# Optimization experiments

Hardware: AMD Instinct MI355X
Metric: run time of the kernel (lower is better)

The kernel has to match this reference:

```python
import jax, jax.numpy as jnp
import numpy as np

N_QUBITS = 256
N_LAYERS = 8
BATCH = 65536


def _ln(h, w, b):
    mu = jnp.mean(h, axis=-1, keepdims=True)
    var = jnp.mean((h - mu) ** 2, axis=-1, keepdims=True)
    return (h - mu) * jax.lax.rsqrt(var + 1e-5) * w + b


def setup_inputs() -> dict:
    key = jax.random.key(0)
    ks = jax.random.split(key, 22)
    Q = N_QUBITS
    s = 0.05
    f = jnp.float32
    return {
        "x": jax.random.normal(ks[0], (BATCH, Q), f),
        # type-0 sublayers (layers 0,3,6): Linear(Q,3Q)+LN+GELU+Linear(3Q,Q)
        "dense0_w1": jax.random.normal(ks[1], (3, Q, 3 * Q), f) * s,
        "dense0_b1": jnp.zeros((3, 3 * Q), f),
        "ln_w": jnp.ones((3, 3 * Q), f),
        "ln_b": jnp.zeros((3, 3 * Q), f),
        "dense0_w2": jax.random.normal(ks[2], (3, 3 * Q, Q), f) * s,
        "dense0_b2": jnp.zeros((3, Q), f),
        # type-1 sublayers (layers 1,4,7): Linear(Q,2Q)+SiLU+Linear(2Q,Q)
        "dense1_w1": jax.random.normal(ks[3], (3, Q, 2 * Q), f) * s,
        "dense1_b1": jnp.zeros((3, 2 * Q), f),
        "dense1_w2": jax.random.normal(ks[4], (3, 2 * Q, Q), f) * s,
        "dense1_b2": jnp.zeros((3, Q), f),
        # attention sublayers (layers 2,5): in_proj (qkv) + out_proj, heads=2, seq_len=1
        "attn_wqkv": jax.random.normal(ks[5], (2, Q, 3 * Q), f) * s,
        "attn_bqkv": jnp.zeros((2, 3 * Q), f),
        "attn_wo": jax.random.normal(ks[6], (2, Q, Q), f) * s,
        "attn_bo": jnp.zeros((2, Q), f),
        # per-layer gate params and entanglement matrices (torch randn init)
        "gate_params": jax.random.normal(ks[7], (N_LAYERS, Q, 6), f),
        "ent": jax.random.normal(ks[8], (N_LAYERS, Q, Q), f) * s,
        # nonlinear ops (4 = n_layers//2): Linear+Tanh+Linear
        "nl_w1": jax.random.normal(ks[9], (4, Q, Q), f) * s,
        "nl_b1": jnp.zeros((4, Q), f),
        "nl_w2": jax.random.normal(ks[10], (4, Q, Q), f) * s,
        "nl_b2": jnp.zeros((4, Q), f),
    }


def _forward(x, dense0_w1, dense0_b1, ln_w, ln_b, dense0_w2, dense0_b2,
             dense1_w1, dense1_b1, dense1_w2, dense1_b2,
             attn_wqkv, attn_bqkv, attn_wo, attn_bo,
             gate_params, ent, nl_w1, nl_b1, nl_w2, nl_b2):
    Q = N_QUBITS
    cur = x
    for li in range(N_LAYERS):
        res = cur
        t = li % 3
        if t == 0:
            i = li // 3
            h = cur @ dense0_w1[i] + dense0_b1[i]
            h = _ln(h, ln_w[i], ln_b[i])
            h = jax.nn.gelu(h, approximate=False)  # torch nn.GELU default (erf)
            cur = h @ dense0_w2[i] + dense0_b2[i]
        elif t == 1:
            i = (li - 1) // 3
            h = jax.nn.silu(cur @ dense1_w1[i] + dense1_b1[i])
            cur = h @ dense1_w2[i] + dense1_b2[i]
        else:
            i = (li - 2) // 3
            # seq_len == 1: softmax over a single key is identically 1, so
            # attended == v; q/k projections contribute zero (incl. gradient).
            qkv = cur @ attn_wqkv[i] + attn_bqkv[i]
            v = qkv[:, 2 * Q:]
            cur = v @ attn_wo[i] + attn_bo[i]
        # fused per-qubit gate effects (vectorized over qubits & batch)
        p = gate_params[li]  # [Q, 6]
        lin = jnp.sin(p[:, 0]) + jnp.cos(p[:, 1]) + jnp.tanh(p[:, 2])  # [Q]
        gate = (lin * cur
                + 0.5 * jnp.sin(p[:, 3] * cur + p[:, 4])
                + 0.5 * jnp.cos(p[:, 5] * cur)) / 4.0
        entangled = cur @ jnp.tanh(ent[li])
        cur = (cur + 0.3 * gate + 0.2 * entangled) / 1.5
        if li % 2 == 1:
            j = li // 2  # 0..3, always < 4 here
            nl = jnp.tanh(cur @ nl_w1[j] + nl_b1[j]) @ nl_w2[j] + nl_b2[j]
            cur = cur + 0.1 * nl
        alpha = 0.8 if li < N_LAYERS // 2 else 0.6
        cur = alpha * cur + (1.0 - alpha) * res
        cur = cur / (jnp.linalg.norm(cur, axis=1, keepdims=True) + 1e-8)
        cur = jnp.tanh(cur)
    return cur


def reference(x, dense0_w1, dense0_b1, ln_w, ln_b, dense0_w2, dense0_b2,
              dense1_w1, dense1_b1, dense1_w2, dense1_b2,
              attn_wqkv, attn_bqkv, attn_wo, attn_bo,
              gate_params, ent, nl_w1, nl_b1, nl_w2, nl_b2):
    return _forward(x, dense0_w1, dense0_b1, ln_w, ln_b, dense0_w2, dense0_b2,
                    dense1_w1, dense1_b1, dense1_w2, dense1_b2,
                    attn_wqkv, attn_bqkv, attn_wo, attn_bo,
                    gate_params, ent, nl_w1, nl_b1, nl_w2, nl_b2)
```

## Files before the change

### kernel.cpp

```cpp
#include <hip/hip_runtime.h>
#include <stdint.h>

#define DI __device__ __forceinline__

typedef __bf16 bf16;
typedef __bf16 bf16x8 __attribute__((ext_vector_type(8)));
typedef float  f32x4  __attribute__((ext_vector_type(4)));

constexpr int Q = 256;
constexpr int BATCH = 65536;
constexpr int TM = 64;
constexpr int THREADS = 512;
constexpr int NW = 8;
constexpr int NBLK = BATCH / TM;
constexpr int SC = Q + 8;

constexpr int W0A_OFF = 0;
constexpr int W0B_OFF = W0A_OFF + 3*768*256;
constexpr int W1A_OFF = W0B_OFF + 3*256*768;
constexpr int W1B_OFF = W1A_OFF + 3*512*256;
constexpr int WV_OFF  = W1B_OFF + 3*256*512;
constexpr int WO_OFF  = WV_OFF  + 2*256*256;
constexpr int ENT_OFF = WO_OFF  + 2*256*256;
constexpr int NL1_OFF = ENT_OFF + 8*256*256;
constexpr int NL2_OFF = NL1_OFF + 4*256*256;
constexpr int WEND    = NL2_OFF + 4*256*256;
constexpr size_t F32_BYTE_OFF = (((size_t)WEND*2) + 255) & ~(size_t)255;

constexpr int P_D0B1 = 0;
constexpr int P_LNW  = P_D0B1 + 3*768;
constexpr int P_LNB  = P_LNW  + 3*768;
constexpr int P_D0B2 = P_LNB  + 3*768;
constexpr int P_D1B1 = P_D0B2 + 3*256;
constexpr int P_D1B2 = P_D1B1 + 3*512;
constexpr int P_BQV  = P_D1B2 + 3*256;
constexpr int P_BO   = P_BQV  + 2*256;
constexpr int P_NB1  = P_BO   + 2*256;
constexpr int P_NB2  = P_NB1  + 4*256;
constexpr int P_GLIN = P_NB2  + 4*256;
constexpr int P_GP3  = P_GLIN + 8*256;
constexpr int P_GP4  = P_GP3  + 8*256;
constexpr int P_GP5  = P_GP4  + 8*256;
constexpr int P_END  = P_GP5  + 8*256;
constexpr size_t FLAG_OFF = F32_BYTE_OFF + (size_t)P_END*4;

DI float ldf(const void* p, size_t idx, int f32) {
  return f32 ? ((const float*)p)[idx] : (float)((const bf16*)p)[idx];
}

DI float tanh_fast(float x) {
  float ax = fabsf(x);
  float e  = __expf(-2.0f * ax);
  float r  = (1.0f - e) / (1.0f + e);
  return copysignf(r, x);
}

DI float gelu_f(float x) {
  float ax = fabsf(x) * 0.70710678118654752f;
  float t  = 1.0f / (1.0f + 0.3275911f * ax);
  float y  = t*(0.254829592f + t*(-0.284496736f + t*(1.421413741f +
             t*(-1.453152027f + t*1.061405429f))));
  float er = copysignf(1.0f - y * __expf(-ax*ax), x);
  return 0.5f * x * (1.0f + er);
}

DI f32x4 mfma_bf16(uint4 a, uint4 b, f32x4 c) {
  return __builtin_amdgcn_mfma_f32_16x16x32_bf16(
      __builtin_bit_cast(bf16x8, a), __builtin_bit_cast(bf16x8, b), c, 0, 0, 0);
}

template<int NJ>
DI void zero_acc(f32x4 (&a)[4][NJ]) {
#pragma unroll
  for (int i = 0; i < 4; ++i)
#pragma unroll
    for (int j = 0; j < NJ; ++j) a[i][j] = f32x4{0.f, 0.f, 0.f, 0.f};
}

template<int NJ>
DI void gemm_k256(const bf16* A, const bf16* __restrict__ Bt, int kdb, int koff,
                  f32x4 (&acc)[4][NJ], int wave, int quad, int l16) {
  const bf16* ar[4];
#pragma unroll
  for (int mt = 0; mt < 4; ++mt) ar[mt] = A + (mt*16 + l16)*SC + quad*8;
  const bf16* br[NJ];
#pragma unroll
  for (int nj = 0; nj < NJ; ++nj)
    br[nj] = Bt + (size_t)((nj*NW + wave)*16 + l16)*kdb + koff + quad*8;
#pragma unroll
  for (int ks = 0; ks < 8; ++ks) {
    uint4 av[4];
#pragma unroll
    for (int mt = 0; mt < 4; ++mt) av[mt] = *(const uint4*)(ar[mt] + ks*32);
#pragma unroll
    for (int nj = 0; nj < NJ; ++nj) {
      uint4 bv = *(const uint4*)(br[nj] + ks*32);
#pragma unroll
      for (int mt = 0; mt < 4; ++mt) acc[mt][nj] = mfma_bf16(av[mt], bv, acc[mt][nj]);
    }
  }
}

template<int NJ>
DI void gemm_k256r(const bf16* A, const bf16* __restrict__ Bt, int kdb, int koff,
                   f32x4 (&acc)[4][NJ], int wave, int quad, int l16) {
  const bf16* ar[4];
#pragma unroll
  for (int mt = 0; mt < 4; ++mt) ar[mt] = A + (mt*16 + l16)*SC + quad*8;
  const bf16* br[NJ];
#pragma unroll
  for (int nj = 0; nj < NJ; ++nj)
    br[nj] = Bt + (size_t)((nj*NW + wave)*16 + l16)*kdb + koff + quad*8;
#pragma unroll
  for (int ks = 7; ks >= 0; --ks) {
    uint4 av[4];
#pragma unroll
    for (int mt = 0; mt < 4; ++mt) av[mt] = *(const uint4*)(ar[mt] + ks*32);
#pragma unroll
    for (int nj = 0; nj < NJ; ++nj) {
      uint4 bv = *(const uint4*)(br[nj] + ks*32);
#pragma unroll
      for (int mt = 0; mt < 4; ++mt) acc[mt][nj] = mfma_bf16(av[mt], bv, acc[mt][nj]);
    }
  }
}

template<int NJ>
DI void addbias(f32x4 (&a)[4][NJ], const float* __restrict__ b, int wave, int l16) {
#pragma unroll
  for (int nj = 0; nj < NJ; ++nj) {
    float bb = b[(nj*NW + wave)*16 + l16];
#pragma unroll
    for (int mt = 0; mt < 4; ++mt)
#pragma unroll
      for (int reg = 0; reg < 4; ++reg) a[mt][nj][reg] += bb;
  }
}

template<int NJ>
DI void store_t(bf16* dst, const f32x4 (&a)[4][NJ], int wave, int quad, int l16) {
#pragma unroll
  for (int nj = 0; nj < NJ; ++nj) {
    int col = (nj*NW + wave)*16 + l16;
#pragma unroll
    for (int mt = 0; mt < 4; ++mt)
#pragma unroll
      for (int reg = 0; reg < 4; ++reg)
        dst[(mt*16 + quad*4 + reg)*SC + col] = (bf16)a[mt][nj][reg];
  }
}

__global__ void detect_dtype(const uint16_t* __restrict__ xr, int* __restrict__ flag) {
  __shared__ int s_max;
  if (threadIdx.x == 0) s_max = 0;
  __syncthreads();
  int e = 0;
  for (int i = threadIdx.x; i < 4096; i += 256) {
    int ex = (xr[2*i] >> 7) & 0xFF;
    e = e > ex ? e : ex;
  }
  atomicMax(&s_max, e);
  __syncthreads();
  if (threadIdx.x == 0) *flag = (s_max >= 140) ? 1 : 0;
}

__global__ void pack_weights(const void* __restrict__ d0w1, const void* __restrict__ d0w2,
                             const void* __restrict__ d1w1, const void* __restrict__ d1w2,
                             const void* __restrict__ wqkv, const void* __restrict__ wo,
                             const void* __restrict__ ent,  const void* __restrict__ nl1,
                             const void* __restrict__ nl2,  bf16* __restrict__ wsb,
                             const int* __restrict__ flag) {
  const int f32 = *flag;
  int job = blockIdx.y;
  const void* src; int mi, K, N, srcN, col0 = 0, dtanh = 0; long dst;
  if      (job < 3)  { src=d0w1; mi=job;    K=256; N=768; srcN=768; dst=W0A_OFF + (long)mi*768*256; }
  else if (job < 6)  { src=d0w2; mi=job-3;  K=768; N=256; srcN=256; dst=W0B_OFF + (long)mi*256*768; }
  else if (job < 9)  { src=d1w1; mi=job-6;  K=256; N=512; srcN=512; dst=W1A_OFF + (long)mi*512*256; }
  else if (job < 12) { src=d1w2; mi=job-9;  K=512; N=256; srcN=256; dst=W1B_OFF + (long)mi*256*512; }
  else if (job < 14) { src=wqkv; mi=job-12; K=256; N=256; srcN=768; col0=512; dst=WV_OFF + (long)mi*65536; }
  else if (job < 16) { src=wo;   mi=job-14; K=256; N=256; srcN=256; dst=WO_OFF + (long)mi*65536; }
  else if (job < 24) { src=ent;  mi=job-16; K=256; N=256; srcN=256; dst=ENT_OFF + (long)mi*65536; dtanh=1; }
  else if (job < 28) { src=nl1;  mi=job-24; K=256; N=256; srcN=256; dst=NL1_OFF + (long)mi*65536; }
  else               { src=nl2;  mi=job-28; K=256; N=256; srcN=256; dst=NL2_OFF + (long)mi*65536; }
  const size_t base = (size_t)mi * K * srcN;

  int tk = K/64, tn = N/64;
  int tile = blockIdx.x;
  if (tile >= tk*tn) return;
  int ik = tile % tk, in_ = tile / tk;

  __shared__ float t[64][65];
  int tid = threadIdx.x;
  for (int e = tid; e < 4096; e += 256) {
    int r = e >> 6, c = e & 63;
    t[r][c] = ldf(src, base + (size_t)(ik*64 + r)*srcN + col0 + in_*64 + c, f32);
  }
  __syncthreads();
  for (int e = tid; e < 4096; e += 256) {
    int nr = e >> 6, kc = e & 63;
    float v = t[kc][nr];
    if (dtanh) v = tanhf(v);
    wsb[dst + (size_t)(in_*64 + nr)*K + ik*64 + kc] = (bf16)v;
  }
}

__global__ void pack_params(const void* __restrict__ d0b1, const void* __restrict__ lnw,
                            const void* __restrict__ lnb,  const void* __restrict__ d0b2,
                            const void* __restrict__ d1b1, const void* __restrict__ d1b2,
                            const void* __restrict__ bqkv, const void* __restrict__ bo,
                            const void* __restrict__ gp,   const void* __restrict__ nb1,
                            const void* __restrict__ nb2,  float* __restrict__ wsf,
                            const int* __restrict__ flag) {
  const int f32 = *flag;
  int i = blockIdx.x * blockDim.x + threadIdx.x;
  if (i >= P_END) return;
  float v;
  if      (i < P_LNW)  { v = ldf(d0b1, i - P_D0B1, f32); }
  else if (i < P_LNB)  { v = ldf(lnw, i - P_LNW, f32); }
  else if (i < P_D0B2) { v = ldf(lnb, i - P_LNB, f32); }
  else if (i < P_D1B1) { v = ldf(d0b2, i - P_D0B2, f32); }
  else if (i < P_D1B2) { v = ldf(d1b1, i - P_D1B1, f32); }
  else if (i < P_BQV)  { v = ldf(d1b2, i - P_D1B2, f32); }
  else if (i < P_BO)   { int k = i - P_BQV; v = ldf(bqkv, (size_t)(k >> 8)*768 + 512 + (k & 255), f32); }
  else if (i < P_NB1)  { v = ldf(bo, i - P_BO, f32); }
  else if (i < P_NB2)  { v = ldf(nb1, i - P_NB1, f32); }
  else if (i < P_GLIN) { v = ldf(nb2, i - P_NB2, f32); }
  else if (i < P_GP3)  { int k = i - P_GLIN;
                         v = sinf(ldf(gp, (size_t)k*6 + 0, f32)) +
                             cosf(ldf(gp, (size_t)k*6 + 1, f32)) +
                             tanhf(ldf(gp, (size_t)k*6 + 2, f32)); }
  else if (i < P_GP4)  { int k = i - P_GP3; v = ldf(gp, (size_t)k*6 + 3, f32); }
  else if (i < P_GP5)  { int k = i - P_GP4; v = ldf(gp, (size_t)k*6 + 4, f32); }
  else                 { int k = i - P_GP5; v = ldf(gp, (size_t)k*6 + 5, f32); }
  wsf[i] = v;
}

__global__ __launch_bounds__(THREADS, 2)
void vqc_main(const void* __restrict__ x, const bf16* __restrict__ wsb,
              const float* __restrict__ wsf, const int* __restrict__ flag,
              void* __restrict__ out) {
  __shared__ __align__(16) bf16 curT[TM*SC];
  __shared__ __align__(16) bf16 buf0[TM*SC];
  __shared__ float red[2*NW*TM];
  __shared__ float rowa[TM], rowb[TM];

  const int tid  = threadIdx.x;
  const int wave = tid >> 6, lane = tid & 63;
  const int quad = lane >> 4, l16 = lane & 15;
  const size_t rowbase = (size_t)blockIdx.x * TM;
  const int f32io = *flag;

  if (f32io) {
    const float* xf = (const float*)x;
    for (int i = tid; i < TM*Q/4; i += THREADS) {
      int r = i >> 6, c4 = (i & 63) * 4;
      float4 v = *(const float4*)(xf + (rowbase + r)*Q + c4);
      bf16* d = curT + r*SC + c4;
      d[0] = (bf16)v.x; d[1] = (bf16)v.y; d[2] = (bf16)v.z; d[3] = (bf16)v.w;
    }
  } else {
    const bf16* xb = (const bf16*)x;
    for (int i = tid; i < TM*Q/8; i += THREADS) {
      int r = i >> 5, c8 = (i & 31) * 8;
      *(uint4*)(curT + r*SC + c8) = *(const uint4*)(xb + (rowbase + r)*Q + c8);
    }
  }
  __syncthreads();

#pragma unroll 1
  for (int li = 0; li < 8; ++li) {
    const int t = li % 3;
    f32x4 acc2[4][2]; zero_acc<2>(acc2);

    if (t == 0) {
      const int i = li / 3;
      const bf16* w1 = wsb + W0A_OFF + (size_t)i*768*256;
      const bf16* w2 = wsb + W0B_OFF + (size_t)i*256*768;
      const float* b1 = wsf + P_D0B1 + i*768;

      float sa4[4][4], sb4[4][4];
#pragma unroll
      for (int mt = 0; mt < 4; ++mt)
#pragma unroll
        for (int reg = 0; reg < 4; ++reg) { sa4[mt][reg] = 0.f; sb4[mt][reg] = 0.f; }
#pragma unroll 1
      for (int c = 0; c < 3; ++c) {
        f32x4 acs[4][2]; zero_acc<2>(acs);
        gemm_k256r<2>(curT, w1 + (size_t)c*256*256, 256, 0, acs, wave, quad, l16);
#pragma unroll
        for (int njl = 0; njl < 2; ++njl) {
          float bb = b1[c*256 + (njl*NW + wave)*16 + l16];
#pragma unroll
          for (int mt = 0; mt < 4; ++mt)
#pragma unroll
            for (int reg = 0; reg < 4; ++reg) {
              float v = acs[mt][njl][reg] + bb;
              sa4[mt][reg] += v; sb4[mt][reg] += v*v;
            }
        }
      }
#pragma unroll
      for (int mt = 0; mt < 4; ++mt) {
#pragma unroll
        for (int reg = 0; reg < 4; ++reg) {
          float sa = sa4[mt][reg], sb = sb4[mt][reg];
#pragma unroll
          for (int m = 1; m < 16; m <<= 1) { sa += __shfl_xor(sa, m, 64); sb += __shfl_xor(sb, m, 64); }
          if (l16 == 0) {
            int row = mt*16 + quad*4 + reg;
            red[wave*TM + row] = sa; red[NW*TM + wave*TM + row] = sb;
          }
        }
      }
      __syncthreads();
      if (tid < TM) {
        float sa = 0.f, sb = 0.f;
#pragma unroll
        for (int w = 0; w < NW; ++w) { sa += red[w*TM + tid]; sb += red[NW*TM + w*TM + tid]; }
        float mu  = sa * (1.0f/768.0f);
        float var = sb * (1.0f/768.0f) - mu*mu;
        rowa[tid] = mu; rowb[tid] = rsqrtf(fmaxf(var, 0.f) + 1e-5f);
      }
      __syncthreads();

#pragma unroll 1
      for (int c = 0; c < 3; ++c) {
        f32x4 acs[4][2]; zero_acc<2>(acs);
        gemm_k256<2>(curT, w1 + (size_t)c*256*256, 256, 0, acs, wave, quad, l16);
        const float* lw = wsf + P_LNW + i*768 + c*256;
        const float* lb = wsf + P_LNB + i*768 + c*256;
#pragma unroll
        for (int njl = 0; njl < 2; ++njl) {
          int col = (njl*NW + wave)*16 + l16;
          float bb = b1[c*256 + col];
          float w_ = lw[col], lbb = lb[col];
#pragma unroll
          for (int mt = 0; mt < 4; ++mt)
#pragma unroll
            for (int reg = 0; reg < 4; ++reg) {
              int row = mt*16 + quad*4 + reg;
              float h = gelu_f((acs[mt][njl][reg] + bb - rowa[row]) * rowb[row] * w_ + lbb);
              buf0[row*SC + col] = (bf16)h;
            }
        }
        __syncthreads();
        gemm_k256<2>(buf0, w2, 768, 256*c, acc2, wave, quad, l16);
        __syncthreads();
      }
      addbias<2>(acc2, wsf + P_D0B2 + i*256, wave, l16);
    } else if (t == 1) {
      const int i = (li - 1) / 3;
      const bf16* w1 = wsb + W1A_OFF + (size_t)i*512*256;
      const bf16* w2 = wsb + W1B_OFF + (size_t)i*256*512;
      const float* b1 = wsf + P_D1B1 + i*512;
#pragma unroll 1
      for (int c = 0; c < 2; ++c) {
        f32x4 acs[4][2]; zero_acc<2>(acs);
        gemm_k256<2>(curT, w1 + (size_t)c*256*256, 256, 0, acs, wave, quad, l16);
#pragma unroll
        for (int njl = 0; njl < 2; ++njl) {
          int col = (njl*NW + wave)*16 + l16;
          float bb = b1[c*256 + col];
#pragma unroll
          for (int mt = 0; mt < 4; ++mt)
#pragma unroll
            for (int reg = 0; reg < 4; ++reg) {
              float xv = acs[mt][njl][reg] + bb;
              buf0[(mt*16 + quad*4 + reg)*SC + col] = (bf16)(xv / (1.0f + __expf(-xv)));
            }
        }
        __syncthreads();
        gemm_k256<2>(buf0, w2, 512, 256*c, acc2, wave, quad, l16);
        __syncthreads();
      }
      addbias<2>(acc2, wsf + P_D1B2 + i*256, wave, l16);
    } else {
      const int i = (li - 2) / 3;
      f32x4 acc[4][2]; zero_acc<2>(acc);
      gemm_k256<2>(curT, wsb + WV_OFF + (size_t)i*65536, 256, 0, acc, wave, quad, l16);
      addbias<2>(acc, wsf + P_BQV + i*256, wave, l16);
      store_t<2>(buf0, acc, wave, quad, l16);
      __syncthreads();
      gemm_k256<2>(buf0, wsb + WO_OFF + (size_t)i*65536, 256, 0, acc2, wave, quad, l16);
      addbias<2>(acc2, wsf + P_BO + i*256, wave, l16);
      __syncthreads();
    }

    store_t<2>(buf0, acc2, wave, quad, l16);
    __syncthreads();
    f32x4 acc3[4][2]; zero_acc<2>(acc3);
    gemm_k256<2>(buf0, wsb + ENT_OFF + (size_t)li*65536, 256, 0, acc3, wave, quad, l16);
    __syncthreads();

    const float* gl = wsf + P_GLIN + li*256;
    const float* g3 = wsf + P_GP3  + li*256;
    const float* g4 = wsf + P_GP4  + li*256;
    const float* g5 = wsf + P_GP5  + li*256;
#pragma unroll
    for (int nj = 0; nj < 2; ++nj) {
      int col = (nj*NW + wave)*16 + l16;
      float lin = gl[col], p3 = g3[col], p4 = g4[col], p5 = g5[col];
#pragma unroll
      for (int mt = 0; mt < 4; ++mt)
#pragma unroll
        for (int reg = 0; reg < 4; ++reg) {
          float v = acc2[mt][nj][reg];
          float gate = (lin*v + 0.5f*__sinf(p3*v + p4) + 0.5f*__cosf(p5*v)) * 0.25f;
          acc2[mt][nj][reg] = (v + 0.3f*gate + 0.2f*acc3[mt][nj][reg]) * (1.0f/1.5f);
        }
    }

    if (li & 1) {
      const int j = li >> 1;
      store_t<2>(buf0, acc2, wave, quad, l16);
      __syncthreads();
      f32x4 a4[4][2]; zero_acc<2>(a4);
      gemm_k256<2>(buf0, wsb + NL1_OFF + (size_t)j*65536, 256, 0, a4, wave, quad, l16);
      const float* nb1p = wsf + P_NB1 + j*256;
      __syncthreads();
#pragma unroll
      for (int nj = 0; nj < 2; ++nj) {
        int col = (nj*NW + wave)*16 + l16;
        float bb = nb1p[col];
#pragma unroll
        for (int mt = 0; mt < 4; ++mt)
#pragma unroll
          for (int reg = 0; reg < 4; ++reg)
            buf0[(mt*16 + quad*4 + reg)*SC + col] = (bf16)tanh_fast(a4[mt][nj][reg] + bb);
      }
      __syncthreads();
      f32x4 a5[4][2]; zero_acc<2>(a5);
      gemm_k256<2>(buf0, wsb + NL2_OFF + (size_t)j*65536, 256, 0, a5, wave, quad, l16);
      const float* nb2p = wsf + P_NB2 + j*256;
#pragma unroll
      for (int nj = 0; nj < 2; ++nj) {
        float bb = nb2p[(nj*NW + wave)*16 + l16];
#pragma unroll
        for (int mt = 0; mt < 4; ++mt)
#pragma unroll
          for (int reg = 0; reg < 4; ++reg) acc2[mt][nj][reg] += 0.1f*(a5[mt][nj][reg] + bb);
      }
    }

    const float alpha = (li < 4) ? 0.8f : 0.6f;
    const float beta  = 1.0f - alpha;
#pragma unroll
    for (int nj = 0; nj < 2; ++nj) {
      int col = (nj*NW + wave)*16 + l16;
#pragma unroll
      for (int mt = 0; mt < 4; ++mt)
#pragma unroll
        for (int reg = 0; reg < 4; ++reg) {
          int row = mt*16 + quad*4 + reg;
          acc2[mt][nj][reg] = alpha*acc2[mt][nj][reg] + beta*(float)curT[row*SC + col];
        }
    }
#pragma unroll
    for (int mt = 0; mt < 4; ++mt) {
#pragma unroll
      for (int reg = 0; reg < 4; ++reg) {
        float s = 0.f;
#pragma unroll
        for (int nj = 0; nj < 2; ++nj) s += acc2[mt][nj][reg]*acc2[mt][nj][reg];
#pragma unroll
        for (int m = 1; m < 16; m <<= 1) s += __shfl_xor(s, m, 64);
        if (l16 == 0) red[wave*TM + mt*16 + quad*4 + reg] = s;
      }
    }
    __syncthreads();
    if (tid < TM) {
      float s = 0.f;
#pragma unroll
      for (int w = 0; w < NW; ++w) s += red[w*TM + tid];
      rowa[tid] = 1.0f / (sqrtf(fmaxf(s, 0.f)) + 1e-8f);
    }
    __syncthreads();
#pragma unroll
    for (int nj = 0; nj < 2; ++nj) {
      int col = (nj*NW + wave)*16 + l16;
#pragma unroll
      for (int mt = 0; mt < 4; ++mt)
#pragma unroll
        for (int reg = 0; reg < 4; ++reg) {
          int row = mt*16 + quad*4 + reg;
          curT[row*SC + col] = (bf16)tanh_fast(acc2[mt][nj][reg] * rowa[row]);
        }
    }
    __syncthreads();
  }

  if (f32io) {
    float* of = (float*)out;
    for (int i = tid; i < TM*Q/4; i += THREADS) {
      int r = i >> 6, c4 = (i & 63) * 4;
      const bf16* s = curT + r*SC + c4;
      float4 v = make_float4((float)s[0], (float)s[1], (float)s[2], (float)s[3]);
      *(float4*)(of + (rowbase + r)*Q + c4) = v;
    }
  } else {
    bf16* ob = (bf16*)out;
    for (int i = tid; i < TM*Q/8; i += THREADS) {
      int r = i >> 5, c8 = (i & 31) * 8;
      *(uint4*)(ob + (rowbase + r)*Q + c8) = *(const uint4*)(curT + r*SC + c8);
    }
  }
}

extern "C" void kernel_launch(void* const* d_in, const int* in_sizes, int n_in,
                              void* d_out, int out_size, void* d_ws, size_t ws_size,
                              hipStream_t stream) {
  const void* x    = d_in[0];
  const void* d0w1 = d_in[1];
  const void* d0b1 = d_in[2];
  const void* lnw  = d_in[3];
  const void* lnb  = d_in[4];
  const void* d0w2 = d_in[5];
  const void* d0b2 = d_in[6];
  const void* d1w1 = d_in[7];
  const void* d1b1 = d_in[8];
  const void* d1w2 = d_in[9];
  const void* d1b2 = d_in[10];
  const void* wqkv = d_in[11];
  const void* bqkv = d_in[12];
  const void* wo   = d_in[13];
  const void* bo   = d_in[14];
  const void* gp   = d_in[15];
  const void* ent  = d_in[16];
  const void* nl1  = d_in[17];
  const void* nb1  = d_in[18];
  const void* nl2  = d_in[19];
  const void* nb2  = d_in[20];

  bf16*  wsb  = (bf16*)d_ws;
  float* wsf  = (float*)((char*)d_ws + F32_BYTE_OFF);
  int*   flag = (int*)((char*)d_ws + FLAG_OFF);

  detect_dtype<<<dim3(1), dim3(256), 0, stream>>>((const uint16_t*)x, flag);
  pack_weights<<<dim3(48, 32), dim3(256), 0, stream>>>(
      d0w1, d0w2, d1w1, d1w2, wqkv, wo, ent, nl1, nl2, wsb, flag);
  pack_params<<<dim3((P_END + 255)/256), dim3(256), 0, stream>>>(
      d0b1, lnw, lnb, d0b2, d1b1, d1b2, bqkv, bo, gp, nb1, nb2, wsf, flag);
  vqc_main<<<dim3(NBLK), dim3(THREADS), 0, stream>>>(x, wsb, wsf, flag, d_out);
}
```

Baseline: 1.701 ms.

## Precompose entanglement and attention weights into second-layer GEMMs on device

Adds small preprocessing kernels that multiply each sublayer's output weight matrix by the tanh(ent) matrix, and compose the attention V and O projections into one matrix. The per-layer GEMM then produces both the sublayer output and its entangled product in one wider pass with concatenated weights. This removes the separate entanglement GEMM, its LDS store/sync round trip, and one attention GEMM per batch tile. In exchange the accumulators double in size, which raises register pressure, and pre-multiplying the weights in bf16 changes rounding.

Result: slower. 1.903 ms (+11.9%).

```diff
diff --git a/kernel.cpp b/kernel.cpp
--- a/kernel.cpp
+++ b/kernel.cpp
@@ -17,14 +17,15 @@
 
 constexpr int W0A_OFF = 0;
 constexpr int W0B_OFF = W0A_OFF + 3*768*256;
-constexpr int W1A_OFF = W0B_OFF + 3*256*768;
+constexpr int W1A_OFF = W0B_OFF + 3*512*768;
 constexpr int W1B_OFF = W1A_OFF + 3*512*256;
-constexpr int WV_OFF  = W1B_OFF + 3*256*512;
-constexpr int WO_OFF  = WV_OFF  + 2*256*256;
-constexpr int ENT_OFF = WO_OFF  + 2*256*256;
-constexpr int NL1_OFF = ENT_OFF + 8*256*256;
-constexpr int NL2_OFF = NL1_OFF + 4*256*256;
-constexpr int WEND    = NL2_OFF + 4*256*256;
+constexpr int WV_OFF  = W1B_OFF + 3*512*512;
+constexpr int WO_OFF  = WV_OFF  + 2*65536;
+constexpr int ATF_OFF = WO_OFF  + 2*65536;
+constexpr int ENT_OFF = ATF_OFF + 2*512*256;
+constexpr int NL1_OFF = ENT_OFF + 8*65536;
+constexpr int NL2_OFF = NL1_OFF + 4*65536;
+constexpr int WEND    = NL2_OFF + 4*65536;
 constexpr size_t F32_BYTE_OFF = (((size_t)WEND*2) + 255) & ~(size_t)255;
 
 constexpr int P_D0B1 = 0;
@@ -41,8 +42,11 @@
 constexpr int P_GP3  = P_GLIN + 8*256;
 constexpr int P_GP4  = P_GP3  + 8*256;
 constexpr int P_GP5  = P_GP4  + 8*256;
-constexpr int P_END  = P_GP5  + 8*256;
-constexpr size_t FLAG_OFF = F32_BYTE_OFF + (size_t)P_END*4;
+constexpr int P_PACK_END = P_GP5 + 8*256;
+constexpr int P_BAT  = P_PACK_END;
+constexpr int P_BENT = P_BAT + 2*256;
+constexpr int P_TOT  = P_BENT + 8*256;
+constexpr size_t FLAG_OFF = F32_BYTE_OFF + (size_t)P_TOT*4;
 
 DI float ldf(const void* p, size_t idx, int f32) {
   return f32 ? ((const float*)p)[idx] : (float)((const bf16*)p)[idx];
@@ -125,15 +129,15 @@
   }
 }
 
-template<int NJ>
-DI void addbias(f32x4 (&a)[4][NJ], const float* __restrict__ b, int wave, int l16) {
-#pragma unroll
-  for (int nj = 0; nj < NJ; ++nj) {
+DI void addbias_h(f32x4 (&a)[4][4], const float* __restrict__ b, int njoff,
+                  int wave, int l16) {
+#pragma unroll
+  for (int nj = 0; nj < 2; ++nj) {
     float bb = b[(nj*NW + wave)*16 + l16];
 #pragma unroll
     for (int mt = 0; mt < 4; ++mt)
 #pragma unroll
-      for (int reg = 0; reg < 4; ++reg) a[mt][nj][reg] += bb;
+      for (int reg = 0; reg < 4; ++reg) a[mt][nj + njoff][reg] += bb;
   }
 }
 
@@ -141,6 +145,18 @@
 DI void store_t(bf16* dst, const f32x4 (&a)[4][NJ], int wave, int quad, int l16) {
 #pragma unroll
   for (int nj = 0; nj < NJ; ++nj) {
+    int col = (nj*NW + wave)*16 + l16;
+#pragma unroll
+    for (int mt = 0; mt < 4; ++mt)
+#pragma unroll
+      for (int reg = 0; reg < 4; ++reg)
+        dst[(mt*16 + quad*4 + reg)*SC + col] = (bf16)a[mt][nj][reg];
+  }
+}
+
+DI void store_half(bf16* dst, const f32x4 (&a)[4][4], int wave, int quad, int l16) {
+#pragma unroll
+  for (int nj = 0; nj < 2; ++nj) {
     int col = (nj*NW + wave)*16 + l16;
 #pragma unroll
     for (int mt = 0; mt < 4; ++mt)
@@ -174,9 +190,9 @@
   int job = blockIdx.y;
   const void* src; int mi, K, N, srcN, col0 = 0, dtanh = 0; long dst;
   if      (job < 3)  { src=d0w1; mi=job;    K=256; N=768; srcN=768; dst=W0A_OFF + (long)mi*768*256; }
-  else if (job < 6)  { src=d0w2; mi=job-3;  K=768; N=256; srcN=256; dst=W0B_OFF + (long)mi*256*768; }
+  else if (job < 6)  { src=d0w2; mi=job-3;  K=768; N=256; srcN=256; dst=W0B_OFF + (long)mi*512*768; }
   else if (job < 9)  { src=d1w1; mi=job-6;  K=256; N=512; srcN=512; dst=W1A_OFF + (long)mi*512*256; }
-  else if (job < 12) { src=d1w2; mi=job-9;  K=512; N=256; srcN=256; dst=W1B_OFF + (long)mi*256*512; }
+  else if (job < 12) { src=d1w2; mi=job-9;  K=512; N=256; srcN=256; dst=W1B_OFF + (long)mi*512*512; }
   else if (job < 14) { src=wqkv; mi=job-12; K=256; N=256; srcN=768; col0=512; dst=WV_OFF + (long)mi*65536; }
   else if (job < 16) { src=wo;   mi=job-14; K=256; N=256; srcN=256; dst=WO_OFF + (long)mi*65536; }
   else if (job < 24) { src=ent;  mi=job-16; K=256; N=256; srcN=256; dst=ENT_OFF + (long)mi*65536; dtanh=1; }
@@ -213,7 +229,7 @@
                             const int* __restrict__ flag) {
   const int f32 = *flag;
   int i = blockIdx.x * blockDim.x + threadIdx.x;
-  if (i >= P_END) return;
+  if (i >= P_PACK_END) return;
   float v;
   if      (i < P_LNW)  { v = ldf(d0b1, i - P_D0B1, f32); }
   else if (i < P_LNB)  { v = ldf(lnw, i - P_LNW, f32); }
@@ -235,6 +251,64 @@
   wsf[i] = v;
 }
 
+__global__ void fuse_gemm(bf16* __restrict__ wsb, int stage) {
+  int job = blockIdx.z;
+  const bf16 *A, *B; bf16* C; int KB;
+  if (stage == 0) {
+    if (job < 2) {
+      A = wsb + WO_OFF + (size_t)job*65536;
+      B = wsb + WV_OFF + (size_t)job*65536;
+      C = wsb + ATF_OFF + (size_t)job*512*256; KB = 256;
+    } else if (job < 5) {
+      int i = job - 2;
+      A = wsb + ENT_OFF + (size_t)(3*i)*65536;
+      B = wsb + W0B_OFF + (size_t)i*512*768;
+      C = wsb + W0B_OFF + (size_t)i*512*768 + 256*768; KB = 768;
+    } else {
+      int i = job - 5;
+      A = wsb + ENT_OFF + (size_t)(3*i + 1)*65536;
+      B = wsb + W1B_OFF + (size_t)i*512*512;
+      C = wsb + W1B_OFF + (size_t)i*512*512 + 256*512; KB = 512;
+    }
+  } else {
+    int i = job;
+    A = wsb + ENT_OFF + (size_t)(3*i + 2)*65536;
+    B = wsb + ATF_OFF + (size_t)i*512*256;
+    C = wsb + ATF_OFF + (size_t)i*512*256 + 256*256; KB = 256;
+  }
+  int m = blockIdx.x * 256 + threadIdx.x;
+  if (m >= KB) return;
+  int c = blockIdx.y;
+  float s = 0.f;
+  for (int n = 0; n < 256; ++n) s += (float)A[c*256 + n] * (float)B[(size_t)n*KB + m];
+  C[(size_t)c*KB + m] = (bf16)s;
+}
+
+__global__ void fuse_bias(const bf16* __restrict__ wsb, float* __restrict__ wsf, int stage) {
+  int t = blockIdx.x * blockDim.x + threadIdx.x;
+  if (stage == 0) {
+    if (t >= 512) return;
+    int i = t >> 8, c = t & 255;
+    const float* bqv = wsf + P_BQV + i*256;
+    const bf16* woT = wsb + WO_OFF + (size_t)i*65536;
+    float s = wsf[P_BO + i*256 + c];
+    for (int m = 0; m < 256; ++m) s += bqv[m] * (float)woT[c*256 + m];
+    wsf[P_BAT + i*256 + c] = s;
+  } else {
+    if (t >= 2048) return;
+    int li = t >> 8, c = t & 255;
+    int tt = li % 3;
+    const float* b2;
+    if (tt == 0)      b2 = wsf + P_D0B2 + (li/3)*256;
+    else if (tt == 1) b2 = wsf + P_D1B2 + ((li-1)/3)*256;
+    else              b2 = wsf + P_BAT  + ((li-2)/3)*256;
+    const bf16* Et = wsb + ENT_OFF + (size_t)li*65536;
+    float s = 0.f;
+    for (int n = 0; n < 256; ++n) s += b2[n] * (float)Et[c*256 + n];
+    wsf[P_BENT + li*256 + c] = s;
+  }
+}
+
 __global__ __launch_bounds__(THREADS, 2)
 void vqc_main(const void* __restrict__ x, const bf16* __restrict__ wsb,
               const float* __restrict__ wsf, const int* __restrict__ flag,
@@ -270,12 +344,12 @@
 #pragma unroll 1
   for (int li = 0; li < 8; ++li) {
     const int t = li % 3;
-    f32x4 acc2[4][2]; zero_acc<2>(acc2);
+    f32x4 acc4[4][4]; zero_acc<4>(acc4);
 
     if (t == 0) {
       const int i = li / 3;
-      const bf16* w1 = wsb + W0A_OFF + (size_t)i*768*256;
-      const bf16* w2 = wsb + W0B_OFF + (size_t)i*256*768;
+      const bf16* w1  = wsb + W0A_OFF + (size_t)i*768*256;
+      const bf16* w2c = wsb + W0B_OFF + (size_t)i*512*768;
       const float* b1 = wsf + P_D0B1 + i*768;
 
       float sa4[4][4], sb4[4][4];
@@ -344,14 +418,15 @@
             }
         }
         __syncthreads();
-        gemm_k256<2>(buf0, w2, 768, 256*c, acc2, wave, quad, l16);
+        gemm_k256<4>(buf0, w2c, 768, 256*c, acc4, wave, quad, l16);
         __syncthreads();
       }
-      addbias<2>(acc2, wsf + P_D0B2 + i*256, wave, l16);
+      addbias_h(acc4, wsf + P_D0B2 + i*256, 0, wave, l16);
+      addbias_h(acc4, wsf + P_BENT + li*256, 2, wave, l16);
     } else if (t == 1) {
       const int i = (li - 1) / 3;
-      const bf16* w1 = wsb + W1A_OFF + (size_t)i*512*256;
-      const bf16* w2 = wsb + W1B_OFF + (size_t)i*256*512;
+      const bf16* w1  = wsb + W1A_OFF + (size_t)i*512*256;
+      const bf16* w2c = wsb + W1B_OFF + (size_t)i*512*512;
       const float* b1 = wsf + P_D1B1 + i*512;
 #pragma unroll 1
       for (int c = 0; c < 2; ++c) {
@@ -370,27 +445,17 @@
             }
         }
         __syncthreads();
-        gemm_k256<2>(buf0, w2, 512, 256*c, acc2, wave, quad, l16);
+        gemm_k256<4>(buf0, w2c, 512, 256*c, acc4, wave, quad, l16);
         __syncthreads();
       }
-      addbias<2>(acc2, wsf + P_D1B2 + i*256, wave, l16);
+      addbias_h(acc4, wsf + P_D1B2 + i*256, 0, wave, l16);
+      addbias_h(acc4, wsf + P_BENT + li*256, 2, wave, l16);
     } else {
       const int i = (li - 2) / 3;
-      f32x4 acc[4][2]; zero_acc<2>(acc);
-      gemm_k256<2>(curT, wsb + WV_OFF + (size_t)i*65536, 256, 0, acc, wave, quad, l16);
-      addbias<2>(acc, wsf + P_BQV + i*256, wave, l16);
-      store_t<2>(buf0, acc, wave, quad, l16);
-      __syncthreads();
-      gemm_k256<2>(buf0, wsb + WO_OFF + (size_t)i*65536, 256, 0, acc2, wave, quad, l16);
-      addbias<2>(acc2, wsf + P_BO + i*256, wave, l16);
-      __syncthreads();
-    }
-
-    store_t<2>(buf0, acc2, wave, quad, l16);
-    __syncthreads();
-    f32x4 acc3[4][2]; zero_acc<2>(acc3);
-    gemm_k256<2>(buf0, wsb + ENT_OFF + (size_t)li*65536, 256, 0, acc3, wave, quad, l16);
-    __syncthreads();
+      gemm_k256<4>(curT, wsb + ATF_OFF + (size_t)i*512*256, 256, 0, acc4, wave, quad, l16);
+      addbias_h(acc4, wsf + P_BAT  + i*256, 0, wave, l16);
+      addbias_h(acc4, wsf + P_BENT + li*256, 2, wave, l16);
+    }
 
     const float* gl = wsf + P_GLIN + li*256;
     const float* g3 = wsf + P_GP3  + li*256;
@@ -404,15 +469,15 @@
       for (int mt = 0; mt < 4; ++mt)
 #pragma unroll
         for (int reg = 0; reg < 4; ++reg) {
-          float v = acc2[mt][nj][reg];
+          float v = acc4[mt][nj][reg];
           float gate = (lin*v + 0.5f*__sinf(p3*v + p4) + 0.5f*__cosf(p5*v)) * 0.25f;
-          acc2[mt][nj][reg] = (v + 0.3f*gate + 0.2f*acc3[mt][nj][reg]) * (1.0f/1.5f);
+          acc4[mt][nj][reg] = (v + 0.3f*gate + 0.2f*acc4[mt][nj+2][reg]) * (1.0f/1.5f);
         }
     }
 
     if (li & 1) {
       const int j = li >> 1;
-      store_t<2>(buf0, acc2, wave, quad, l16);
+      store_half(buf0, acc4, wave, quad, l16);
       __syncthreads();
       f32x4 a4[4][2]; zero_acc<2>(a4);
       gemm_k256<2>(buf0, wsb + NL1_OFF + (size_t)j*65536, 256, 0, a4, wave, quad, l16);
@@ -438,7 +503,7 @@
 #pragma unroll
         for (int mt = 0; mt < 4; ++mt)
 #pragma unroll
-          for (int reg = 0; reg < 4; ++reg) acc2[mt][nj][reg] += 0.1f*(a5[mt][nj][reg] + bb);
+          for (int reg = 0; reg < 4; ++reg) acc4[mt][nj][reg] += 0.1f*(a5[mt][nj][reg] + bb);
       }
     }
 
@@ -452,7 +517,7 @@
 #pragma unroll
         for (int reg = 0; reg < 4; ++reg) {
           int row = mt*16 + quad*4 + reg;
-          acc2[mt][nj][reg] = alpha*acc2[mt][nj][reg] + beta*(float)curT[row*SC + col];
+          acc4[mt][nj][reg] = alpha*acc4[mt][nj][reg] + beta*(float)curT[row*SC + col];
         }
     }
 #pragma unroll
@@ -461,7 +526,7 @@
       for (int reg = 0; reg < 4; ++reg) {
         float s = 0.f;
 #pragma unroll
-        for (int nj = 0; nj < 2; ++nj) s += acc2[mt][nj][reg]*acc2[mt][nj][reg];
+        for (int nj = 0; nj < 2; ++nj) s += acc4[mt][nj][reg]*acc4[mt][nj][reg];
 #pragma unroll
         for (int m = 1; m < 16; m <<= 1) s += __shfl_xor(s, m, 64);
         if (l16 == 0) red[wave*TM + mt*16 + quad*4 + reg] = s;
@@ -483,7 +548,7 @@
 #pragma unroll
         for (int reg = 0; reg < 4; ++reg) {
           int row = mt*16 + quad*4 + reg;
-          curT[row*SC + col] = (bf16)tanh_fast(acc2[mt][nj][reg] * rowa[row]);
+          curT[row*SC + col] = (bf16)tanh_fast(acc4[mt][nj][reg] * rowa[row]);
         }
     }
     __syncthreads();
@@ -538,7 +603,11 @@
   detect_dtype<<<dim3(1), dim3(256), 0, stream>>>((const uint16_t*)x, flag);
   pack_weights<<<dim3(48, 32), dim3(256), 0, stream>>>(
       d0w1, d0w2, d1w1, d1w2, wqkv, wo, ent, nl1, nl2, wsb, flag);
-  pack_params<<<dim3((P_END + 255)/256), dim3(256), 0, stream>>>(
+  pack_params<<<dim3((P_PACK_END + 255)/256), dim3(256), 0, stream>>>(
       d0b1, lnw, lnb, d0b2, d1b1, d1b2, bqkv, bo, gp, nb1, nb2, wsf, flag);
+  fuse_gemm<<<dim3(3, 256, 8), dim3(256), 0, stream>>>(wsb, 0);
+  fuse_gemm<<<dim3(1, 256, 2), dim3(256), 0, stream>>>(wsb, 1);
+  fuse_bias<<<dim3(2), dim3(256), 0, stream>>>(wsb, wsf, 0);
+  fuse_bias<<<dim3(8), dim3(256), 0, stream>>>(wsb, wsf, 1);
   vqc_main<<<dim3(NBLK), dim3(THREADS), 0, stream>>>(x, wsb, wsf, flag, d_out);
 }
```

## Fold attention V and out projections into one matrix and double row tile

Applied to the files above, without the earlier changes.

With sequence length one, attention reduces to out_proj(V(x)), so the two weight matrices are multiplied once in a small preprocessing kernel along with a fused bias. The main kernel then does one GEMM per attention layer instead of two, plus a sync and a bf16 round trip through shared memory. The row tile per block also doubles from 64 to 128 (MT=8), so each loaded weight fragment feeds twice as many MFMAs. The cost is double the accumulator registers per thread, which may cause spills or cut occupancy under launch_bounds(512,2), plus an extra bf16 rounding of the fused weight.

Result: faster. 1.559 ms (-8.3%).

```diff
diff --git a/kernel.cpp b/kernel.cpp
--- a/kernel.cpp
+++ b/kernel.cpp
@@ -9,9 +9,10 @@
 
 constexpr int Q = 256;
 constexpr int BATCH = 65536;
-constexpr int TM = 64;
+constexpr int TM = 128;
 constexpr int THREADS = 512;
 constexpr int NW = 8;
+constexpr int MT = 8;
 constexpr int NBLK = BATCH / TM;
 constexpr int SC = Q + 8;
 
@@ -20,11 +21,12 @@
 constexpr int W1A_OFF = W0B_OFF + 3*256*768;
 constexpr int W1B_OFF = W1A_OFF + 3*512*256;
 constexpr int WV_OFF  = W1B_OFF + 3*256*512;
-constexpr int WO_OFF  = WV_OFF  + 2*256*256;
-constexpr int ENT_OFF = WO_OFF  + 2*256*256;
-constexpr int NL1_OFF = ENT_OFF + 8*256*256;
-constexpr int NL2_OFF = NL1_OFF + 4*256*256;
-constexpr int WEND    = NL2_OFF + 4*256*256;
+constexpr int WO_OFF  = WV_OFF  + 2*65536;
+constexpr int ATF_OFF = WO_OFF  + 2*65536;
+constexpr int ENT_OFF = ATF_OFF + 2*65536;
+constexpr int NL1_OFF = ENT_OFF + 8*65536;
+constexpr int NL2_OFF = NL1_OFF + 4*65536;
+constexpr int WEND    = NL2_OFF + 4*65536;
 constexpr size_t F32_BYTE_OFF = (((size_t)WEND*2) + 255) & ~(size_t)255;
 
 constexpr int P_D0B1 = 0;
@@ -41,8 +43,10 @@
 constexpr int P_GP3  = P_GLIN + 8*256;
 constexpr int P_GP4  = P_GP3  + 8*256;
 constexpr int P_GP5  = P_GP4  + 8*256;
-constexpr int P_END  = P_GP5  + 8*256;
-constexpr size_t FLAG_OFF = F32_BYTE_OFF + (size_t)P_END*4;
+constexpr int P_PACK_END = P_GP5 + 8*256;
+constexpr int P_BAT  = P_PACK_END;
+constexpr int P_TOT  = P_BAT + 2*256;
+constexpr size_t FLAG_OFF = F32_BYTE_OFF + (size_t)P_TOT*4;
 
 DI float ldf(const void* p, size_t idx, int f32) {
   return f32 ? ((const float*)p)[idx] : (float)((const bf16*)p)[idx];
@@ -70,80 +74,80 @@
 }
 
 template<int NJ>
-DI void zero_acc(f32x4 (&a)[4][NJ]) {
-#pragma unroll
-  for (int i = 0; i < 4; ++i)
+DI void zero_acc(f32x4 (&a)[MT][NJ]) {
+#pragma unroll
+  for (int i = 0; i < MT; ++i)
 #pragma unroll
     for (int j = 0; j < NJ; ++j) a[i][j] = f32x4{0.f, 0.f, 0.f, 0.f};
 }
 
 template<int NJ>
 DI void gemm_k256(const bf16* A, const bf16* __restrict__ Bt, int kdb, int koff,
-                  f32x4 (&acc)[4][NJ], int wave, int quad, int l16) {
-  const bf16* ar[4];
-#pragma unroll
-  for (int mt = 0; mt < 4; ++mt) ar[mt] = A + (mt*16 + l16)*SC + quad*8;
+                  f32x4 (&acc)[MT][NJ], int wave, int quad, int l16) {
+  const bf16* ar[MT];
+#pragma unroll
+  for (int mt = 0; mt < MT; ++mt) ar[mt] = A + (mt*16 + l16)*SC + quad*8;
   const bf16* br[NJ];
 #pragma unroll
   for (int nj = 0; nj < NJ; ++nj)
     br[nj] = Bt + (size_t)((nj*NW + wave)*16 + l16)*kdb + koff + quad*8;
 #pragma unroll
   for (int ks = 0; ks < 8; ++ks) {
-    uint4 av[4];
-#pragma unroll
-    for (int mt = 0; mt < 4; ++mt) av[mt] = *(const uint4*)(ar[mt] + ks*32);
+    uint4 av[MT];
+#pragma unroll
+    for (int mt = 0; mt < MT; ++mt) av[mt] = *(const uint4*)(ar[mt] + ks*32);
 #pragma unroll
     for (int nj = 0; nj < NJ; ++nj) {
       uint4 bv = *(const uint4*)(br[nj] + ks*32);
 #pragma unroll
-      for (int mt = 0; mt < 4; ++mt) acc[mt][nj] = mfma_bf16(av[mt], bv, acc[mt][nj]);
+      for (int mt = 0; mt < MT; ++mt) acc[mt][nj] = mfma_bf16(av[mt], bv, acc[mt][nj]);
     }
   }
 }
 
 template<int NJ>
 DI void gemm_k256r(const bf16* A, const bf16* __restrict__ Bt, int kdb, int koff,
-                   f32x4 (&acc)[4][NJ], int wave, int quad, int l16) {
-  const bf16* ar[4];
-#pragma unroll
-  for (int mt = 0; mt < 4; ++mt) ar[mt] = A + (mt*16 + l16)*SC + quad*8;
+                   f32x4 (&acc)[MT][NJ], int wave, int quad, int l16) {
+  const bf16* ar[MT];
+#pragma unroll
+  for (int mt = 0; mt < MT; ++mt) ar[mt] = A + (mt*16 + l16)*SC + quad*8;
   const bf16* br[NJ];
 #pragma unroll
   for (int nj = 0; nj < NJ; ++nj)
     br[nj] = Bt + (size_t)((nj*NW + wave)*16 + l16)*kdb + koff + quad*8;
 #pragma unroll
   for (int ks = 7; ks >= 0; --ks) {
-    uint4 av[4];
-#pragma unroll
-    for (int mt = 0; mt < 4; ++mt) av[mt] = *(const uint4*)(ar[mt] + ks*32);
+    uint4 av[MT];
+#pragma unroll
+    for (int mt = 0; mt < MT; ++mt) av[mt] = *(const uint4*)(ar[mt] + ks*32);
 #pragma unroll
     for (int nj = 0; nj < NJ; ++nj) {
       uint4 bv = *(const uint4*)(br[nj] + ks*32);
 #pragma unroll
-      for (int mt = 0; mt < 4; ++mt) acc[mt][nj] = mfma_bf16(av[mt], bv, acc[mt][nj]);
+      for (int mt = 0; mt < MT; ++mt) acc[mt][nj] = mfma_bf16(av[mt], bv, acc[mt][nj]);
     }
   }
 }
 
 template<int NJ>
-DI void addbias(f32x4 (&a)[4][NJ], const float* __restrict__ b, int wave, int l16) {
+DI void addbias(f32x4 (&a)[MT][NJ], const float* __restrict__ b, int wave, int l16) {
 #pragma unroll
   for (int nj = 0; nj < NJ; ++nj) {
     float bb = b[(nj*NW + wave)*16 + l16];
 #pragma unroll
-    for (int mt = 0; mt < 4; ++mt)
+    for (int mt = 0; mt < MT; ++mt)
 #pragma unroll
       for (int reg = 0; reg < 4; ++reg) a[mt][nj][reg] += bb;
   }
 }
 
 template<int NJ>
-DI void store_t(bf16* dst, const f32x4 (&a)[4][NJ], int wave, int quad, int l16) {
+DI void store_t(bf16* dst, const f32x4 (&a)[MT][NJ], int wave, int quad, int l16) {
 #pragma unroll
   for (int nj = 0; nj < NJ; ++nj) {
     int col = (nj*NW + wave)*16 + l16;
 #pragma unroll
-    for (int mt = 0; mt < 4; ++mt)
+    for (int mt = 0; mt < MT; ++mt)
 #pragma unroll
       for (int reg = 0; reg < 4; ++reg)
         dst[(mt*16 + quad*4 + reg)*SC + col] = (bf16)a[mt][nj][reg];
@@ -213,7 +217,7 @@
                             const int* __restrict__ flag) {
   const int f32 = *flag;
   int i = blockIdx.x * blockDim.x + threadIdx.x;
-  if (i >= P_END) return;
+  if (i >= P_PACK_END) return;
   float v;
   if      (i < P_LNW)  { v = ldf(d0b1, i - P_D0B1, f32); }
   else if (i < P_LNB)  { v = ldf(lnw, i - P_LNW, f32); }
@@ -235,6 +239,29 @@
   wsf[i] = v;
 }
 
+__global__ void fuse_gemm(bf16* __restrict__ wsb) {
+  int i = blockIdx.z;
+  const bf16* A = wsb + WO_OFF + (size_t)i*65536;
+  const bf16* B = wsb + WV_OFF + (size_t)i*65536;
+  bf16* C = wsb + ATF_OFF + (size_t)i*65536;
+  int m = threadIdx.x;
+  int c = blockIdx.y;
+  float s = 0.f;
+  for (int n = 0; n < 256; ++n) s += (float)A[c*256 + n] * (float)B[(size_t)n*256 + m];
+  C[(size_t)c*256 + m] = (bf16)s;
+}
+
+__global__ void fuse_bias(const bf16* __restrict__ wsb, float* __restrict__ wsf) {
+  int t = blockIdx.x * blockDim.x + threadIdx.x;
+  if (t >= 512) return;
+  int i = t >> 8, c = t & 255;
+  const float* bqv = wsf + P_BQV + i*256;
+  const bf16* woT = wsb + WO_OFF + (size_t)i*65536;
+  float s = wsf[P_BO + i*256 + c];
+  for (int m = 0; m < 256; ++m) s += bqv[m] * (float)woT[c*256 + m];
+  wsf[P_BAT + i*256 + c] = s;
+}
+
 __global__ __launch_bounds__(THREADS, 2)
 void vqc_main(const void* __restrict__ x, const bf16* __restrict__ wsb,
               const float* __restrict__ wsf, const int* __restrict__ flag,
@@ -270,7 +297,7 @@
 #pragma unroll 1
   for (int li = 0; li < 8; ++li) {
     const int t = li % 3;
-    f32x4 acc2[4][2]; zero_acc<2>(acc2);
+    f32x4 acc2[MT][2];
 
     if (t == 0) {
       const int i = li / 3;
@@ -278,20 +305,20 @@
       const bf16* w2 = wsb + W0B_OFF + (size_t)i*256*768;
       const float* b1 = wsf + P_D0B1 + i*768;
 
-      float sa4[4][4], sb4[4][4];
-#pragma unroll
-      for (int mt = 0; mt < 4; ++mt)
+      float sa4[MT][4], sb4[MT][4];
+#pragma unroll
+      for (int mt = 0; mt < MT; ++mt)
 #pragma unroll
         for (int reg = 0; reg < 4; ++reg) { sa4[mt][reg] = 0.f; sb4[mt][reg] = 0.f; }
 #pragma unroll 1
       for (int c = 0; c < 3; ++c) {
-        f32x4 acs[4][2]; zero_acc<2>(acs);
+        f32x4 acs[MT][2]; zero_acc<2>(acs);
         gemm_k256r<2>(curT, w1 + (size_t)c*256*256, 256, 0, acs, wave, quad, l16);
 #pragma unroll
         for (int njl = 0; njl < 2; ++njl) {
           float bb = b1[c*256 + (njl*NW + wave)*16 + l16];
 #pragma unroll
-          for (int mt = 0; mt < 4; ++mt)
+          for (int mt = 0; mt < MT; ++mt)
 #pragma unroll
             for (int reg = 0; reg < 4; ++reg) {
               float v = acs[mt][njl][reg] + bb;
@@ -300,7 +327,7 @@
         }
       }
 #pragma unroll
-      for (int mt = 0; mt < 4; ++mt) {
+      for (int mt = 0; mt < MT; ++mt) {
 #pragma unroll
         for (int reg = 0; reg < 4; ++reg) {
           float sa = sa4[mt][reg], sb = sb4[mt][reg];
@@ -323,9 +350,10 @@
       }
       __syncthreads();
 
+      zero_acc<2>(acc2);
 #pragma unroll 1
       for (int c = 0; c < 3; ++c) {
-        f32x4 acs[4][2]; zero_acc<2>(acs);
+        f32x4 acs[MT][2]; zero_acc<2>(acs);
         gemm_k256<2>(curT, w1 + (size_t)c*256*256, 256, 0, acs, wave, quad, l16);
         const float* lw = wsf + P_LNW + i*768 + c*256;
         const float* lb = wsf + P_LNB + i*768 + c*256;
@@ -335,7 +363,7 @@
           float bb = b1[c*256 + col];
           float w_ = lw[col], lbb = lb[col];
 #pragma unroll
-          for (int mt = 0; mt < 4; ++mt)
+          for (int mt = 0; mt < MT; ++mt)
 #pragma unroll
             for (int reg = 0; reg < 4; ++reg) {
               int row = mt*16 + quad*4 + reg;
@@ -353,16 +381,17 @@
       const bf16* w1 = wsb + W1A_OFF + (size_t)i*512*256;
       const bf16* w2 = wsb + W1B_OFF + (size_t)i*256*512;
       const float* b1 = wsf + P_D1B1 + i*512;
+      zero_acc<2>(acc2);
 #pragma unroll 1
       for (int c = 0; c < 2; ++c) {
-        f32x4 acs[4][2]; zero_acc<2>(acs);
+        f32x4 acs[MT][2]; zero_acc<2>(acs);
         gemm_k256<2>(curT, w1 + (size_t)c*256*256, 256, 0, acs, wave, quad, l16);
 #pragma unroll
         for (int njl = 0; njl < 2; ++njl) {
           int col = (njl*NW + wave)*16 + l16;
           float bb = b1[c*256 + col];
 #pragma unroll
-          for (int mt = 0; mt < 4; ++mt)
+          for (int mt = 0; mt < MT; ++mt)
 #pragma unroll
             for (int reg = 0; reg < 4; ++reg) {
               float xv = acs[mt][njl][reg] + bb;
@@ -376,19 +405,14 @@
       addbias<2>(acc2, wsf + P_D1B2 + i*256, wave, l16);
     } else {
       const int i = (li - 2) / 3;
-      f32x4 acc[4][2]; zero_acc<2>(acc);
-      gemm_k256<2>(curT, wsb + WV_OFF + (size_t)i*65536, 256, 0, acc, wave, quad, l16);
-      addbias<2>(acc, wsf + P_BQV + i*256, wave, l16);
-      store_t<2>(buf0, acc, wave, quad, l16);
-      __syncthreads();
-      gemm_k256<2>(buf0, wsb + WO_OFF + (size_t)i*65536, 256, 0, acc2, wave, quad, l16);
-      addbias<2>(acc2, wsf + P_BO + i*256, wave, l16);
-      __syncthreads();
+      zero_acc<2>(acc2);
+      gemm_k256<2>(curT, wsb + ATF_OFF + (size_t)i*65536, 256, 0, acc2, wave, quad, l16);
+      addbias<2>(acc2, wsf + P_BAT + i*256, wave, l16);
     }
 
     store_t<2>(buf0, acc2, wave, quad, l16);
     __syncthreads();
-    f32x4 acc3[4][2]; zero_acc<2>(acc3);
+    f32x4 acc3[MT][2]; zero_acc<2>(acc3);
     gemm_k256<2>(buf0, wsb + ENT_OFF + (size_t)li*65536, 256, 0, acc3, wave, quad, l16);
     __syncthreads();
 
@@ -401,7 +425,7 @@
       int col = (nj*NW + wave)*16 + l16;
       float lin = gl[col], p3 = g3[col], p4 = g4[col], p5 = g5[col];
 #pragma unroll
-      for (int mt = 0; mt < 4; ++mt)
+      for (int mt = 0; mt < MT; ++mt)
 #pragma unroll
         for (int reg = 0; reg < 4; ++reg) {
           float v = acc2[mt][nj][reg];
@@ -414,7 +438,7 @@
       const int j = li >> 1;
       store_t<2>(buf0, acc2, wave, quad, l16);
       __syncthreads();
-      f32x4 a4[4][2]; zero_acc<2>(a4);
+      f32x4 a4[MT][2]; zero_acc<2>(a4);
       gemm_k256<2>(buf0, wsb + NL1_OFF + (size_t)j*65536, 256, 0, a4, wave, quad, l16);
       const float* nb1p = wsf + P_NB1 + j*256;
       __syncthreads();
@@ -423,20 +447,20 @@
         int col = (nj*NW + wave)*16 + l16;
         float bb = nb1p[col];
 #pragma unroll
-        for (int mt = 0; mt < 4; ++mt)
+        for (int mt = 0; mt < MT; ++mt)
 #pragma unroll
           for (int reg = 0; reg < 4; ++reg)
             buf0[(mt*16 + quad*4 + reg)*SC + col] = (bf16)tanh_fast(a4[mt][nj][reg] + bb);
       }
       __syncthreads();
-      f32x4 a5[4][2]; zero_acc<2>(a5);
+      f32x4 a5[MT][2]; zero_acc<2>(a5);
       gemm_k256<2>(buf0, wsb + NL2_OFF + (size_t)j*65536, 256, 0, a5, wave, quad, l16);
       const float* nb2p = wsf + P_NB2 + j*256;
 #pragma unroll
       for (int nj = 0; nj < 2; ++nj) {
         float bb = nb2p[(nj*NW + wave)*16 + l16];
 #pragma unroll
-        for (int mt = 0; mt < 4; ++mt)
+        for (int mt = 0; mt < MT; ++mt)
 #pragma unroll
           for (int reg = 0; reg < 4; ++reg) acc2[mt][nj][reg] += 0.1f*(a5[mt][nj][reg] + bb);
       }
@@ -448,7 +472,7 @@
     for (int nj = 0; nj < 2; ++nj) {
       int col = (nj*NW + wave)*16 + l16;
 #pragma unroll
-      for (int mt = 0; mt < 4; ++mt)
+      for (int mt = 0; mt < MT; ++mt)
 #pragma unroll
         for (int reg = 0; reg < 4; ++reg) {
           int row = mt*16 + quad*4 + reg;
@@ -456,7 +480,7 @@
         }
     }
 #pragma unroll
-    for (int mt = 0; mt < 4; ++mt) {
+    for (int mt = 0; mt < MT; ++mt) {
 #pragma unroll
       for (int reg = 0; reg < 4; ++reg) {
         float s = 0.f;
@@ -479,7 +503,7 @@
     for (int nj = 0; nj < 2; ++nj) {
       int col = (nj*NW + wave)*16 + l16;
 #pragma unroll
-      for (int mt = 0; mt < 4; ++mt)
+      for (int mt = 0; mt < MT; ++mt)
 #pragma unroll
         for (int reg = 0; reg < 4; ++reg) {
           int row = mt*16 + quad*4 + reg;
@@ -538,7 +562,9 @@
   detect_dtype<<<dim3(1), dim3(256), 0, stream>>>((const uint16_t*)x, flag);
   pack_weights<<<dim3(48, 32), dim3(256), 0, stream>>>(
       d0w1, d0w2, d1w1, d1w2, wqkv, wo, ent, nl1, nl2, wsb, flag);
-  pack_params<<<dim3((P_END + 255)/256), dim3(256), 0, stream>>>(
+  pack_params<<<dim3((P_PACK_END + 255)/256), dim3(256), 0, stream>>>(
       d0b1, lnw, lnb, d0b2, d1b1, d1b2, bqkv, bo, gp, nb1, nb2, wsf, flag);
+  fuse_gemm<<<dim3(1, 256, 2), dim3(256), 0, stream>>>(wsb);
+  fuse_bias<<<dim3(2), dim3(256), 0, stream>>>(wsb, wsf);
   vqc_main<<<dim3(NBLK), dim3(THREADS), 0, stream>>>(x, wsb, wsf, flag, d_out);
 }
```
